# Kernel optimization log

Hardware: AMD Instinct MI355X
Metric: run time of the kernel (lower is better)

Reference implementation:

```python
import jax, jax.numpy as jnp
import numpy as np

B, T, V, H, E, MAX_OOV = 128, 200, 50257, 256, 128, 50


def setup_inputs() -> dict:
    key = jax.random.key(0)
    ks = jax.random.split(key, 17)
    s = 0.05  # param scale
    return {
        "decoder_input": jax.random.randint(ks[0], (B, 1), 0, V),
        "encoder_outputs": jax.random.normal(ks[1], (B, T, 2 * H), jnp.float32),
        "encoder_idxs": jax.random.randint(ks[2], (B, T), 0, V),
        "prev_state": jax.random.normal(ks[3], (1, B, H), jnp.float32),
        "selective_read": jax.random.normal(ks[4], (B, 1, 2 * H), jnp.float32) * s,
        "step": 1,
        "emb": jax.random.normal(ks[5], (V, E), jnp.float32) * s,
        "W_ih": jax.random.normal(ks[6], (3 * H, E + 2 * H), jnp.float32) * s,
        "W_hh": jax.random.normal(ks[7], (3 * H, H), jnp.float32) * s,
        "b_ih": jax.random.normal(ks[8], (3 * H,), jnp.float32) * s,
        "b_hh": jax.random.normal(ks[9], (3 * H,), jnp.float32) * s,
        "Wi_w": jax.random.normal(ks[10], (H, 2 * H), jnp.float32) * s,
        "Wi_b": jax.random.normal(ks[11], (H,), jnp.float32) * s,
        "Wg_w": jax.random.normal(ks[12], (V, H), jnp.float32) * s,
        "Wg_b": jax.random.normal(ks[13], (V,), jnp.float32) * s,
        "Wc_w": jax.random.normal(ks[14], (H, 2 * H), jnp.float32) * s,
        "Wc_b": jax.random.normal(ks[15], (H,), jnp.float32) * s,
    }


def _gru_cell(x, h, W_ih, W_hh, b_ih, b_hh):
    # torch GRUCell math, gate order r,z,n
    gi = x @ W_ih.T + b_ih
    gh = h @ W_hh.T + b_hh
    i_r, i_z, i_n = jnp.split(gi, 3, axis=-1)
    h_r, h_z, h_n = jnp.split(gh, 3, axis=-1)
    r = jax.nn.sigmoid(i_r + h_r)
    z = jax.nn.sigmoid(i_z + h_z)
    n = jnp.tanh(i_n + r * h_n)
    return (1.0 - z) * n + z * h


def reference(decoder_input, encoder_outputs, encoder_idxs, prev_state, selective_read,
              step, emb, W_ih, W_hh, b_ih, b_hh, Wi_w, Wi_b, Wg_w, Wg_b, Wc_w, Wc_b):
    dtype = encoder_outputs.dtype
    if step == 0:
        prev_state = (encoder_outputs[:, -1] @ Wi_w.T + Wi_b)[None]      # 1,B,H
        selective_read = jnp.zeros((B, 1, 2 * H), dtype)
    embedded = emb[decoder_input[:, 0]]                                   # B,E
    gru_in = jnp.concatenate([selective_read[:, 0], embedded], axis=-1)   # B,2H+E
    decode_hidden = _gru_cell(gru_in, prev_state[0], W_ih, W_hh, b_ih, b_hh)  # B,H

    score_g = decode_hidden @ Wg_w.T + Wg_b                               # B,V
    enc_proj = jnp.tanh(jnp.einsum('bte,he->bth', encoder_outputs, Wc_w) + Wc_b)  # B,T,H
    score_c = jnp.tanh(jnp.einsum('bth,bh->bt', enc_proj, decode_hidden))         # B,T
    score_c = score_c + jnp.where(encoder_idxs == 0, -10000.0, 0.0).astype(dtype)

    probs = jax.nn.softmax(jnp.concatenate([score_g, score_c], axis=1), axis=1)   # B,V+T
    prob_g, prob_c = probs[:, :V], probs[:, V:]
    prob_g = jnp.concatenate([prob_g, jnp.full((B, MAX_OOV), 1e-4, dtype)], axis=1)  # B,V+oov

    # copy-distribution aggregation: scatter-add prob_c by vocab id (replaces one-hot bmm)
    prob_c_to_g = jnp.zeros((B, V + MAX_OOV), dtype).at[
        jnp.arange(B)[:, None], encoder_idxs].add(prob_c)
    prob_out = (prob_c_to_g + prob_g)[:, None, :]                          # B,1,V+oov

    # selective read for next step
    match = (encoder_idxs == decoder_input).astype(dtype)                  # B,T
    tot = match.sum(axis=1, keepdims=True)
    match = jnp.where(tot > 1, match / tot, match)
    prob_appeared = prob_c * match
    selective_read_new = jnp.einsum('bt,bte->be', prob_appeared, encoder_outputs)[:, None, :]  # B,1,2H
    return prob_out, decode_hidden, selective_read_new
```

## Files before the change

kernel.cpp:

```cpp
#include <hip/hip_runtime.h>

typedef __bf16 bf16;
typedef __bf16 bf16x4 __attribute__((ext_vector_type(4)));
typedef __bf16 bf16x8 __attribute__((ext_vector_type(8)));
typedef float f32x4 __attribute__((ext_vector_type(4)));

#define B_ 128
#define T_ 200
#define V_ 50257
#define H_ 256
#define E_ 128
#define OOV_ 50
#define VO_ 50307
#define NRG 64
#define NTS 4
#define GSC 786
#define PSTR 800
#define GPJ 400

__device__ __forceinline__ float sigmoid_(float x) { return 1.0f / (1.0f + __expf(-x)); }
__device__ __forceinline__ float tanh_(float x) { return 1.0f - 2.0f / (__expf(2.0f * x) + 1.0f); }

__global__ void k_front(const float* Wc_w, bf16* WcPack,
                        const int* step_p, const float* enc, const float* prev,
                        const float* selread, const int* dec, const float* emb,
                        const float* Wi_w, const float* Wi_b,
                        float* hT, float* ginT) {
    if (blockIdx.x < 128) {
        int gid = blockIdx.x * 256 + threadIdx.x;
        int n = gid >> 7;
        int k = (gid & 127) * 4;
        float4 v = *(const float4*)(Wc_w + n * 512 + k);
        int kstep = k >> 5, kin = k & 31;
        int q = kin >> 3, j0 = kin & 7;
        int r = n & 15, nt = n >> 4;
        int lane = q * 16 + r;
        bf16* d = WcPack + (((nt * 16 + kstep) * 64) + lane) * 8 + j0;
        d[0] = (bf16)v.x; d[1] = (bf16)v.y; d[2] = (bf16)v.z; d[3] = (bf16)v.w;
    } else {
        int b = blockIdx.x - 128, t = threadIdx.x;
        int step = step_p[0];
        float h;
        if (step == 0) {
            float acc = Wi_b[t];
            const float* er = enc + (b * T_ + (T_ - 1)) * 512;
            const float* wr = Wi_w + t * 512;
            for (int k = 0; k < 512; ++k) acc += er[k] * wr[k];
            h = acc;
        } else {
            h = prev[b * H_ + t];
        }
        hT[t * B_ + b] = h;
        for (int k = t; k < 512; k += 256)
            ginT[k * B_ + b] = (step == 0) ? 0.0f : selread[b * 512 + k];
        if (t < E_)
            ginT[(512 + t) * B_ + b] = emb[dec[b] * E_ + t];
    }
}

__global__ void k_gemm_gru(const float* W_ih, const float* b_ih,
                           const float* W_hh, const float* b_hh,
                           const float* ginT, const float* hT,
                           float* giT, float* ghT) {
    __shared__ float red[256];
    int rrow = blockIdx.x;
    int t = threadIdx.x;
    int b = t & 127, kh = t >> 7;
    const float* w = W_ih + rrow * 640 + kh * 320;
    const float* g = ginT + (kh * 320) * B_ + b;
    float a0 = 0.f, a1 = 0.f, a2 = 0.f, a3 = 0.f;
#pragma unroll 4
    for (int k = 0; k < 320; k += 4) {
        a0 += w[k]     * g[k * B_];
        a1 += w[k + 1] * g[(k + 1) * B_];
        a2 += w[k + 2] * g[(k + 2) * B_];
        a3 += w[k + 3] * g[(k + 3) * B_];
    }
    const float* w2 = W_hh + rrow * 256 + kh * 128;
    const float* hh = hT + (kh * 128) * B_ + b;
    float c0 = 0.f, c1 = 0.f, c2 = 0.f, c3 = 0.f;
#pragma unroll 4
    for (int k = 0; k < 128; k += 4) {
        c0 += w2[k]     * hh[k * B_];
        c1 += w2[k + 1] * hh[(k + 1) * B_];
        c2 += w2[k + 2] * hh[(k + 2) * B_];
        c3 += w2[k + 3] * hh[(k + 3) * B_];
    }
    red[t] = ((a0 + a1) + (a2 + a3));
    __syncthreads();
    if (kh == 0) giT[rrow * B_ + b] = b_ih[rrow] + red[b] + red[b + 128];
    __syncthreads();
    red[t] = ((c0 + c1) + (c2 + c3));
    __syncthreads();
    if (kh == 0) ghT[rrow * B_ + b] = b_hh[rrow] + red[b] + red[b + 128];
}

__global__ void k_gru_cell(const float* giT, const float* ghT, const float* hT,
                           float* out_dh, bf16* Apack) {
    int b = blockIdx.x, j = threadIdx.x;
    float ir = giT[j * B_ + b], iz = giT[(256 + j) * B_ + b], in_ = giT[(512 + j) * B_ + b];
    float hr = ghT[j * B_ + b], hz = ghT[(256 + j) * B_ + b], hn = ghT[(512 + j) * B_ + b];
    float hp = hT[j * B_ + b];
    float r = sigmoid_(ir + hr);
    float z = sigmoid_(iz + hz);
    float n = tanh_(in_ + r * hn);
    float h = (1.0f - z) * n + z * hp;
    out_dh[b * H_ + j] = h;
    int mt = b >> 4, rr = b & 15, ks = j >> 5, q = (j >> 3) & 3, jj = j & 7;
    Apack[(((mt * 8 + ks) * 64) + (q * 16 + rr)) * 8 + jj] = (bf16)h;
}

__global__ __launch_bounds__(256, 4) void k_mm(const bf16* Apack, const float* Wg_w,
                                               const float* Wg_b, const float* enc,
                                               const bf16* WcPack, const float* Wc_b,
                                               const float* dh, const int* idxs,
                                               float* out_prob, float* pg_part, float* expc) {
    __shared__ unsigned char smem[34816];
    int tid = threadIdx.x;
    int w = tid >> 6, lane = tid & 63;
    int r = lane & 15, q = lane >> 4;
    if (blockIdx.x < GSC) {
        int blk = blockIdx.x;
        int n0 = blk * NRG;
        bf16* Bs = (bf16*)smem;
        float4 tmp[16];
#pragma unroll
        for (int j = 0; j < 16; ++j) {
            int f = j * 256 + tid;
            int row = f >> 6, c4 = f & 63;
            int n = n0 + row;
            tmp[j] = (n < V_) ? *(const float4*)(Wg_w + n * 256 + c4 * 4)
                              : float4{0.f, 0.f, 0.f, 0.f};
        }
#pragma unroll
        for (int j = 0; j < 16; ++j) {
            int f = j * 256 + tid;
            int row = f >> 6, c4 = f & 63;
            bf16x4 o;
            o[0] = (bf16)tmp[j].x; o[1] = (bf16)tmp[j].y;
            o[2] = (bf16)tmp[j].z; o[3] = (bf16)tmp[j].w;
            *(bf16x4*)(Bs + row * 264 + c4 * 4) = o;
        }
        bf16x8 a[2][8];
#pragma unroll
        for (int p = 0; p < 2; ++p)
#pragma unroll
            for (int ks = 0; ks < 8; ++ks)
                a[p][ks] = *(const bf16x8*)(Apack + ((2 * w + p) * 8 + ks) * 512 + lane * 8);
        __syncthreads();
        f32x4 acc[8];
#pragma unroll
        for (int i = 0; i < 8; ++i) acc[i] = (f32x4){0.f, 0.f, 0.f, 0.f};
#pragma unroll
        for (int ks = 0; ks < 8; ++ks) {
#pragma unroll
            for (int nt = 0; nt < NTS; ++nt) {
                bf16x8 bfr = *(const bf16x8*)(Bs + (nt * 16 + r) * 264 + ks * 32 + q * 8);
                acc[nt * 2]     = __builtin_amdgcn_mfma_f32_16x16x32_bf16(a[0][ks], bfr, acc[nt * 2], 0, 0, 0);
                acc[nt * 2 + 1] = __builtin_amdgcn_mfma_f32_16x16x32_bf16(a[1][ks], bfr, acc[nt * 2 + 1], 0, 0, 0);
            }
        }
        __syncthreads();
        float* Tr = (float*)smem;
        float rsum[2][4];
#pragma unroll
        for (int p = 0; p < 2; ++p)
#pragma unroll
            for (int rg = 0; rg < 4; ++rg) rsum[p][rg] = 0.0f;
#pragma unroll
        for (int nt = 0; nt < NTS; ++nt) {
            int n = n0 + nt * 16 + r;
            bool valid = n < V_;
            float wgb = valid ? Wg_b[n] : 0.0f;
#pragma unroll
            for (int p = 0; p < 2; ++p) {
#pragma unroll
                for (int rg = 0; rg < 4; ++rg) {
                    int row = (2 * w + p) * 16 + q * 4 + rg;
                    float e = valid ? __expf(acc[nt * 2 + p][rg] + wgb) : 0.0f;
                    Tr[row * 68 + nt * 16 + r] = e;
                    rsum[p][rg] += e;
                }
            }
        }
#pragma unroll
        for (int p = 0; p < 2; ++p) {
#pragma unroll
            for (int rg = 0; rg < 4; ++rg) {
                float s = rsum[p][rg];
                s += __shfl_xor(s, 1);
                s += __shfl_xor(s, 2);
                s += __shfl_xor(s, 4);
                s += __shfl_xor(s, 8);
                if (r == 0) {
                    int row = (2 * w + p) * 16 + q * 4 + rg;
                    pg_part[row * PSTR + blk] = s;
                }
            }
        }
        __syncthreads();
        if (blk < GSC - 1) {
#pragma unroll
            for (int rnd = 0; rnd < 8; ++rnd) {
                int f = rnd * 256 + tid;
                int row = f >> 4;
                int c4 = f & 15;
                float4 v = *(const float4*)(Tr + row * 68 + c4 * 4);
                *(float4*)(out_prob + row * VO_ + n0 + c4 * 4) = v;
            }
        } else {
#pragma unroll
            for (int rnd = 0; rnd < 8; ++rnd) {
                int f = rnd * 256 + tid;
                int row = f >> 4;
                int c4 = f & 15;
#pragma unroll
                for (int i = 0; i < 4; ++i) {
                    int n = n0 + c4 * 4 + i;
                    if (n < V_) out_prob[row * VO_ + n] = Tr[row * 68 + c4 * 4 + i];
                }
            }
        }
    } else {
        int pblk = blockIdx.x - GSC;
        int m0 = pblk * 64;
        bf16* As = (bf16*)smem;
        float* sred = (float*)(smem + 33792);
        f32x4 acc[16];
#pragma unroll
        for (int i = 0; i < 16; ++i) acc[i] = (f32x4){0.f, 0.f, 0.f, 0.f};
        for (int half = 0; half < 2; ++half) {
            __syncthreads();
            float4 tmp[16];
#pragma unroll
            for (int j = 0; j < 16; ++j) {
                int f = j * 256 + tid;
                int row = f >> 6, c4 = f & 63;
                tmp[j] = *(const float4*)(enc + (m0 + row) * 512 + half * 256 + c4 * 4);
            }
#pragma unroll
            for (int j = 0; j < 16; ++j) {
                int f = j * 256 + tid;
                int row = f >> 6, c4 = f & 63;
                bf16x4 o;
                o[0] = (bf16)tmp[j].x; o[1] = (bf16)tmp[j].y;
                o[2] = (bf16)tmp[j].z; o[3] = (bf16)tmp[j].w;
                *(bf16x4*)(As + row * 264 + c4 * 4) = o;
            }
            __syncthreads();
#pragma unroll
            for (int ks = 0; ks < 8; ++ks) {
                int kstep = half * 8 + ks;
                bf16x8 bfr[4];
#pragma unroll
                for (int ntl = 0; ntl < 4; ++ntl)
                    bfr[ntl] = *(const bf16x8*)(WcPack + (((w * 4 + ntl) * 16 + kstep) * 64 + lane) * 8);
#pragma unroll
                for (int mt = 0; mt < 4; ++mt) {
                    bf16x8 a = *(const bf16x8*)(As + (mt * 16 + r) * 264 + ks * 32 + q * 8);
#pragma unroll
                    for (int ntl = 0; ntl < 4; ++ntl)
                        acc[mt * 4 + ntl] = __builtin_amdgcn_mfma_f32_16x16x32_bf16(a, bfr[ntl], acc[mt * 4 + ntl], 0, 0, 0);
                }
            }
        }
#pragma unroll
        for (int mt = 0; mt < 4; ++mt) {
#pragma unroll
            for (int rg = 0; rg < 4; ++rg) {
                int rowl = mt * 16 + q * 4 + rg;
                int row = m0 + rowl;
                int b = row / T_;
                float s = 0.0f;
#pragma unroll
                for (int ntl = 0; ntl < 4; ++ntl) {
                    int n = (w * 4 + ntl) * 16 + r;
                    float pv = tanh_(acc[mt * 4 + ntl][rg] + Wc_b[n]);
                    s += pv * dh[b * H_ + n];
                }
                s += __shfl_xor(s, 1);
                s += __shfl_xor(s, 2);
                s += __shfl_xor(s, 4);
                s += __shfl_xor(s, 8);
                if (r == 0) sred[rowl * 4 + w] = s;
            }
        }
        __syncthreads();
        if (tid < 64) {
            float s = sred[tid * 4] + sred[tid * 4 + 1] + sred[tid * 4 + 2] + sred[tid * 4 + 3];
            int row = m0 + tid;
            int b = row / T_, t = row - b * T_;
            float sc = tanh_(s);
            if (idxs[b * T_ + t] == 0) sc -= 10000.0f;
            expc[row] = __expf(sc);
        }
    }
}

__global__ void k_red_scatter(const float* pg_part, const float* expc_, const int* idxs,
                              const int* dec, const float* enc, float* inv_out,
                              float* out_prob, float* out_sel) {
    __shared__ float red[256];
    __shared__ float cf[256];
    int b = blockIdx.x, t = threadIdx.x;
    float s = 0.0f;
    for (int i = t; i < GSC; i += 256) s += pg_part[b * PSTR + i];
    if (t < T_) s += expc_[b * T_ + t];
    red[t] = s;
    __syncthreads();
    for (int k = 128; k > 0; k >>= 1) {
        if (t < k) red[t] += red[t + k];
        __syncthreads();
    }
    float iv = 1.0f / red[0];
    if (t == 0) inv_out[b] = iv;
    __syncthreads();
    int d = dec[b];
    float ec = 0.0f;
    int m = 0;
    if (t < T_) {
        int ix = idxs[b * T_ + t];
        ec = expc_[b * T_ + t];
        atomicAdd(&out_prob[b * VO_ + ix], ec);
        m = (ix == d) ? 1 : 0;
    }
    cf[t] = m ? ec * iv : 0.0f;
    red[t] = m ? 1.0f : 0.0f;
    __syncthreads();
    for (int k = 128; k > 0; k >>= 1) {
        if (t < k) red[t] += red[t + k];
        __syncthreads();
    }
    float tot = red[0];
    float scale = (tot > 1.0f) ? 1.0f / tot : 1.0f;
    float a0 = 0.0f, a1 = 0.0f;
    for (int tt = 0; tt < T_; ++tt) {
        float c = cf[tt];
        if (c != 0.0f) {
            float wgt = c * scale;
            a0 += wgt * enc[(b * T_ + tt) * 512 + t];
            a1 += wgt * enc[(b * T_ + tt) * 512 + t + 256];
        }
    }
    out_sel[b * 512 + t] = a0;
    out_sel[b * 512 + t + 256] = a1;
}

__global__ void k_norm(float* out_prob, const float* inv) {
    int i4 = blockIdx.x * 256 + threadIdx.x;
    if (i4 >= (B_ * VO_ / 4)) return;
    float4 vv = ((const float4*)out_prob)[i4];
    float r[4];
    int base = i4 * 4;
#pragma unroll
    for (int c = 0; c < 4; ++c) {
        int idx = base + c;
        int b = idx / VO_;
        int v = idx - b * VO_;
        float x = (c == 0) ? vv.x : (c == 1) ? vv.y : (c == 2) ? vv.z : vv.w;
        r[c] = (v < V_) ? x * inv[b] : 1e-4f;
    }
    ((float4*)out_prob)[i4] = make_float4(r[0], r[1], r[2], r[3]);
}

extern "C" void kernel_launch(void* const* d_in, const int* in_sizes, int n_in,
                              void* d_out, int out_size, void* d_ws, size_t ws_size,
                              hipStream_t stream) {
    const int*   dec     = (const int*)d_in[0];
    const float* enc     = (const float*)d_in[1];
    const int*   idxs    = (const int*)d_in[2];
    const float* prev    = (const float*)d_in[3];
    const float* selread = (const float*)d_in[4];
    const int*   step_p  = (const int*)d_in[5];
    const float* emb     = (const float*)d_in[6];
    const float* W_ih    = (const float*)d_in[7];
    const float* W_hh    = (const float*)d_in[8];
    const float* b_ih    = (const float*)d_in[9];
    const float* b_hh    = (const float*)d_in[10];
    const float* Wi_w    = (const float*)d_in[11];
    const float* Wi_b    = (const float*)d_in[12];
    const float* Wg_w    = (const float*)d_in[13];
    const float* Wg_b    = (const float*)d_in[14];
    const float* Wc_w    = (const float*)d_in[15];
    const float* Wc_b    = (const float*)d_in[16];

    float* ws     = (float*)d_ws;
    float* hT     = ws;
    float* ginT   = ws + 32768;
    float* giT    = ws + 114688;
    float* ghT    = ws + 212992;
    float* inv    = ws + 311296;
    float* expc   = ws + 311552;
    float* pgp    = ws + 337152;
    bf16*  Apack  = (bf16*)(ws + 741376);
    bf16*  WcPack = (bf16*)(ws + 757760);

    float* out      = (float*)d_out;
    float* out_prob = out;
    float* out_dh   = out + 6439296;
    float* out_sel  = out + 6439296 + 32768;

    k_front<<<256, 256, 0, stream>>>(Wc_w, WcPack, step_p, enc, prev, selread, dec,
                                     emb, Wi_w, Wi_b, hT, ginT);
    k_gemm_gru<<<768, 256, 0, stream>>>(W_ih, b_ih, W_hh, b_hh, ginT, hT, giT, ghT);
    k_gru_cell<<<B_, 256, 0, stream>>>(giT, ghT, hT, out_dh, Apack);
    k_mm<<<GSC + GPJ, 256, 0, stream>>>(Apack, Wg_w, Wg_b, enc, WcPack, Wc_b,
                                        out_dh, idxs, out_prob, pgp, expc);
    k_red_scatter<<<B_, 256, 0, stream>>>(pgp, expc, idxs, dec, enc, inv, out_prob, out_sel);
    k_norm<<<(B_ * VO_ / 4 + 255) / 256, 256, 0, stream>>>(out_prob, inv);
}
```

Baseline: 282.3 us.

## Fuse normalization into scatter kernel and load Wg directly into MFMA fragments

The separate normalization kernel is removed. Each batch row is now split across two blocks in the reduce/scatter kernel, which scatter-adds the copy probabilities into its half of the vocabulary and then rescales that half in place, and also computes half of the selective-read dimensions. The vocabulary GEMM now converts Wg_w straight from global memory into bf16 MFMA B fragments with a one-step register prefetch, skipping the shared-memory staging. It uses 80-row tiles with launch bounds lowered to 3, and writes exp values directly to the output instead of through a shared transpose. This cuts a launch and a full extra pass over the large output, at the cost of uncoalesced scattered stores and more register pressure.

```diff
diff --git a/kernel.cpp b/kernel.cpp
--- a/kernel.cpp
+++ b/kernel.cpp
@@ -12,10 +12,10 @@
 #define E_ 128
 #define OOV_ 50
 #define VO_ 50307
-#define NRG 64
-#define NTS 4
-#define GSC 786
-#define PSTR 800
+#define NRG 80
+#define NTS 5
+#define GSC 629
+#define PSTR 640
 #define GPJ 400
 
 __device__ __forceinline__ float sigmoid_(float x) { return 1.0f / (1.0f + __expf(-x)); }
@@ -110,7 +110,7 @@
     Apack[(((mt * 8 + ks) * 64) + (q * 16 + rr)) * 8 + jj] = (bf16)h;
 }
 
-__global__ __launch_bounds__(256, 4) void k_mm(const bf16* Apack, const float* Wg_w,
+__global__ __launch_bounds__(256, 3) void k_mm(const bf16* Apack, const float* Wg_w,
                                                const float* Wg_b, const float* enc,
                                                const bf16* WcPack, const float* Wc_b,
                                                const float* dh, const int* idxs,
@@ -122,64 +122,68 @@
     if (blockIdx.x < GSC) {
         int blk = blockIdx.x;
         int n0 = blk * NRG;
-        bf16* Bs = (bf16*)smem;
-        float4 tmp[16];
-#pragma unroll
-        for (int j = 0; j < 16; ++j) {
-            int f = j * 256 + tid;
-            int row = f >> 6, c4 = f & 63;
-            int n = n0 + row;
-            tmp[j] = (n < V_) ? *(const float4*)(Wg_w + n * 256 + c4 * 4)
-                              : float4{0.f, 0.f, 0.f, 0.f};
-        }
-#pragma unroll
-        for (int j = 0; j < 16; ++j) {
-            int f = j * 256 + tid;
-            int row = f >> 6, c4 = f & 63;
-            bf16x4 o;
-            o[0] = (bf16)tmp[j].x; o[1] = (bf16)tmp[j].y;
-            o[2] = (bf16)tmp[j].z; o[3] = (bf16)tmp[j].w;
-            *(bf16x4*)(Bs + row * 264 + c4 * 4) = o;
-        }
-        bf16x8 a[2][8];
-#pragma unroll
-        for (int p = 0; p < 2; ++p)
-#pragma unroll
-            for (int ks = 0; ks < 8; ++ks)
-                a[p][ks] = *(const bf16x8*)(Apack + ((2 * w + p) * 8 + ks) * 512 + lane * 8);
-        __syncthreads();
-        f32x4 acc[8];
-#pragma unroll
-        for (int i = 0; i < 8; ++i) acc[i] = (f32x4){0.f, 0.f, 0.f, 0.f};
-#pragma unroll
-        for (int ks = 0; ks < 8; ++ks) {
-#pragma unroll
-            for (int nt = 0; nt < NTS; ++nt) {
-                bf16x8 bfr = *(const bf16x8*)(Bs + (nt * 16 + r) * 264 + ks * 32 + q * 8);
-                acc[nt * 2]     = __builtin_amdgcn_mfma_f32_16x16x32_bf16(a[0][ks], bfr, acc[nt * 2], 0, 0, 0);
-                acc[nt * 2 + 1] = __builtin_amdgcn_mfma_f32_16x16x32_bf16(a[1][ks], bfr, acc[nt * 2 + 1], 0, 0, 0);
-            }
-        }
-        __syncthreads();
-        float* Tr = (float*)smem;
-        float rsum[2][4];
-#pragma unroll
-        for (int p = 0; p < 2; ++p)
-#pragma unroll
-            for (int rg = 0; rg < 4; ++rg) rsum[p][rg] = 0.0f;
+        const float* rp[NTS];
+        bool valid[NTS];
+        int nrow[NTS];
 #pragma unroll
         for (int nt = 0; nt < NTS; ++nt) {
             int n = n0 + nt * 16 + r;
-            bool valid = n < V_;
-            float wgb = valid ? Wg_b[n] : 0.0f;
+            valid[nt] = (n < V_);
+            nrow[nt] = valid[nt] ? n : (V_ - 1);
+            rp[nt] = Wg_w + nrow[nt] * 256 + q * 8;
+        }
+        f32x4 acc[10];
+#pragma unroll
+        for (int i = 0; i < 10; ++i) acc[i] = (f32x4){0.f, 0.f, 0.f, 0.f};
+        float4 vA[NTS], vB[NTS];
+#pragma unroll
+        for (int nt = 0; nt < NTS; ++nt) {
+            vA[nt] = *(const float4*)(rp[nt]);
+            vB[nt] = *(const float4*)(rp[nt] + 4);
+        }
+#pragma unroll
+        for (int ks = 0; ks < 8; ++ks) {
+            bf16x8 bfr[NTS];
+#pragma unroll
+            for (int nt = 0; nt < NTS; ++nt) {
+                float4 va = vA[nt], vb = vB[nt];
+                bfr[nt][0] = (bf16)va.x; bfr[nt][1] = (bf16)va.y;
+                bfr[nt][2] = (bf16)va.z; bfr[nt][3] = (bf16)va.w;
+                bfr[nt][4] = (bf16)vb.x; bfr[nt][5] = (bf16)vb.y;
+                bfr[nt][6] = (bf16)vb.z; bfr[nt][7] = (bf16)vb.w;
+            }
+            if (ks < 7) {
+#pragma unroll
+                for (int nt = 0; nt < NTS; ++nt) {
+                    vA[nt] = *(const float4*)(rp[nt] + (ks + 1) * 32);
+                    vB[nt] = *(const float4*)(rp[nt] + (ks + 1) * 32 + 4);
+                }
+            }
+            bf16x8 a0 = *(const bf16x8*)(Apack + ((2 * w + 0) * 8 + ks) * 512 + lane * 8);
+            bf16x8 a1 = *(const bf16x8*)(Apack + ((2 * w + 1) * 8 + ks) * 512 + lane * 8);
+#pragma unroll
+            for (int nt = 0; nt < NTS; ++nt) {
+                acc[nt * 2]     = __builtin_amdgcn_mfma_f32_16x16x32_bf16(a0, bfr[nt], acc[nt * 2], 0, 0, 0);
+                acc[nt * 2 + 1] = __builtin_amdgcn_mfma_f32_16x16x32_bf16(a1, bfr[nt], acc[nt * 2 + 1], 0, 0, 0);
+            }
+        }
+        float rsum[2][4];
+#pragma unroll
+        for (int p = 0; p < 2; ++p)
+#pragma unroll
+            for (int rg = 0; rg < 4; ++rg) rsum[p][rg] = 0.0f;
+#pragma unroll
+        for (int nt = 0; nt < NTS; ++nt) {
+            float wgb = Wg_b[nrow[nt]];
+            int n = n0 + nt * 16 + r;
 #pragma unroll
             for (int p = 0; p < 2; ++p) {
 #pragma unroll
                 for (int rg = 0; rg < 4; ++rg) {
                     int row = (2 * w + p) * 16 + q * 4 + rg;
-                    float e = valid ? __expf(acc[nt * 2 + p][rg] + wgb) : 0.0f;
-                    Tr[row * 68 + nt * 16 + r] = e;
+                    float e = valid[nt] ? __expf(acc[nt * 2 + p][rg] + wgb) : 0.0f;
                     rsum[p][rg] += e;
+                    if (valid[nt]) out_prob[row * VO_ + n] = e;
                 }
             }
         }
@@ -198,29 +202,6 @@
                 }
             }
         }
-        __syncthreads();
-        if (blk < GSC - 1) {
-#pragma unroll
-            for (int rnd = 0; rnd < 8; ++rnd) {
-                int f = rnd * 256 + tid;
-                int row = f >> 4;
-                int c4 = f & 15;
-                float4 v = *(const float4*)(Tr + row * 68 + c4 * 4);
-                *(float4*)(out_prob + row * VO_ + n0 + c4 * 4) = v;
-            }
-        } else {
-#pragma unroll
-            for (int rnd = 0; rnd < 8; ++rnd) {
-                int f = rnd * 256 + tid;
-                int row = f >> 4;
-                int c4 = f & 15;
-#pragma unroll
-                for (int i = 0; i < 4; ++i) {
-                    int n = n0 + c4 * 4 + i;
-                    if (n < V_) out_prob[row * VO_ + n] = Tr[row * 68 + c4 * 4 + i];
-                }
-            }
-        }
     } else {
         int pblk = blockIdx.x - GSC;
         int m0 = pblk * 64;
@@ -231,21 +212,24 @@
         for (int i = 0; i < 16; ++i) acc[i] = (f32x4){0.f, 0.f, 0.f, 0.f};
         for (int half = 0; half < 2; ++half) {
             __syncthreads();
-            float4 tmp[16];
-#pragma unroll
-            for (int j = 0; j < 16; ++j) {
-                int f = j * 256 + tid;
-                int row = f >> 6, c4 = f & 63;
-                tmp[j] = *(const float4*)(enc + (m0 + row) * 512 + half * 256 + c4 * 4);
-            }
-#pragma unroll
-            for (int j = 0; j < 16; ++j) {
-                int f = j * 256 + tid;
-                int row = f >> 6, c4 = f & 63;
-                bf16x4 o;
-                o[0] = (bf16)tmp[j].x; o[1] = (bf16)tmp[j].y;
-                o[2] = (bf16)tmp[j].z; o[3] = (bf16)tmp[j].w;
-                *(bf16x4*)(As + row * 264 + c4 * 4) = o;
+#pragma unroll
+            for (int ph = 0; ph < 2; ++ph) {
+                float4 tmp[8];
+#pragma unroll
+                for (int j = 0; j < 8; ++j) {
+                    int f = (ph * 8 + j) * 256 + tid;
+                    int row = f >> 6, c4 = f & 63;
+                    tmp[j] = *(const float4*)(enc + (m0 + row) * 512 + half * 256 + c4 * 4);
+                }
+#pragma unroll
+                for (int j = 0; j < 8; ++j) {
+                    int f = (ph * 8 + j) * 256 + tid;
+                    int row = f >> 6, c4 = f & 63;
+                    bf16x4 o;
+                    o[0] = (bf16)tmp[j].x; o[1] = (bf16)tmp[j].y;
+                    o[2] = (bf16)tmp[j].z; o[3] = (bf16)tmp[j].w;
+                    *(bf16x4*)(As + row * 264 + c4 * 4) = o;
+                }
             }
             __syncthreads();
 #pragma unroll
@@ -298,11 +282,12 @@
 }
 
 __global__ void k_red_scatter(const float* pg_part, const float* expc_, const int* idxs,
-                              const int* dec, const float* enc, float* inv_out,
+                              const int* dec, const float* enc,
                               float* out_prob, float* out_sel) {
     __shared__ float red[256];
     __shared__ float cf[256];
-    int b = blockIdx.x, t = threadIdx.x;
+    int b = blockIdx.x >> 1, hf = blockIdx.x & 1;
+    int t = threadIdx.x;
     float s = 0.0f;
     for (int i = t; i < GSC; i += 256) s += pg_part[b * PSTR + i];
     if (t < T_) s += expc_[b * T_ + t];
@@ -313,15 +298,18 @@
         __syncthreads();
     }
     float iv = 1.0f / red[0];
-    if (t == 0) inv_out[b] = iv;
     __syncthreads();
     int d = dec[b];
+    const int halfc = (VO_ + 1) / 2;
+    int cl0 = hf * halfc;
+    int cl1 = (cl0 + halfc < VO_) ? cl0 + halfc : VO_;
     float ec = 0.0f;
     int m = 0;
     if (t < T_) {
         int ix = idxs[b * T_ + t];
         ec = expc_[b * T_ + t];
-        atomicAdd(&out_prob[b * VO_ + ix], ec);
+        if (ix >= cl0 && ix < cl1)
+            atomicAdd(&out_prob[b * VO_ + ix], ec);
         m = (ix == d) ? 1 : 0;
     }
     cf[t] = m ? ec * iv : 0.0f;
@@ -333,34 +321,39 @@
     }
     float tot = red[0];
     float scale = (tot > 1.0f) ? 1.0f / tot : 1.0f;
-    float a0 = 0.0f, a1 = 0.0f;
+    int dim = t + hf * 256;
+    float a0 = 0.0f;
     for (int tt = 0; tt < T_; ++tt) {
         float c = cf[tt];
-        if (c != 0.0f) {
-            float wgt = c * scale;
-            a0 += wgt * enc[(b * T_ + tt) * 512 + t];
-            a1 += wgt * enc[(b * T_ + tt) * 512 + t + 256];
-        }
-    }
-    out_sel[b * 512 + t] = a0;
-    out_sel[b * 512 + t + 256] = a1;
-}
-
-__global__ void k_norm(float* out_prob, const float* inv) {
-    int i4 = blockIdx.x * 256 + threadIdx.x;
-    if (i4 >= (B_ * VO_ / 4)) return;
-    float4 vv = ((const float4*)out_prob)[i4];
-    float r[4];
-    int base = i4 * 4;
-#pragma unroll
-    for (int c = 0; c < 4; ++c) {
-        int idx = base + c;
-        int b = idx / VO_;
-        int v = idx - b * VO_;
-        float x = (c == 0) ? vv.x : (c == 1) ? vv.y : (c == 2) ? vv.z : vv.w;
-        r[c] = (v < V_) ? x * inv[b] : 1e-4f;
-    }
-    ((float4*)out_prob)[i4] = make_float4(r[0], r[1], r[2], r[3]);
+        if (c != 0.0f) a0 += c * scale * enc[(b * T_ + tt) * 512 + dim];
+    }
+    out_sel[b * 512 + dim] = a0;
+    __threadfence();
+    __syncthreads();
+    int base = b * VO_;
+    int s0 = base + cl0, s1 = base + cl1;
+    int a4 = (s0 + 3) & ~3;
+    int b4 = s1 & ~3;
+    if (t < a4 - s0) {
+        int i = s0 + t;
+        int col = i - base;
+        out_prob[i] = (col < V_) ? out_prob[i] * iv : 1e-4f;
+    }
+    if (t < s1 - b4) {
+        int i = b4 + t;
+        int col = i - base;
+        out_prob[i] = (col < V_) ? out_prob[i] * iv : 1e-4f;
+    }
+    for (int i4 = a4 / 4 + t; i4 < b4 / 4; i4 += 256) {
+        float4 v = *(const float4*)(out_prob + i4 * 4);
+        int c0 = i4 * 4 - base;
+        float o[4];
+        o[0] = (c0 + 0 < V_) ? v.x * iv : 1e-4f;
+        o[1] = (c0 + 1 < V_) ? v.y * iv : 1e-4f;
+        o[2] = (c0 + 2 < V_) ? v.z * iv : 1e-4f;
+        o[3] = (c0 + 3 < V_) ? v.w * iv : 1e-4f;
+        *(float4*)(out_prob + i4 * 4) = make_float4(o[0], o[1], o[2], o[3]);
+    }
 }
 
 extern "C" void kernel_launch(void* const* d_in, const int* in_sizes, int n_in,
@@ -389,7 +382,6 @@
     float* ginT   = ws + 32768;
     float* giT    = ws + 114688;
     float* ghT    = ws + 212992;
-    float* inv    = ws + 311296;
     float* expc   = ws + 311552;
     float* pgp    = ws + 337152;
     bf16*  Apack  = (bf16*)(ws + 741376);
@@ -406,6 +398,5 @@
     k_gru_cell<<<B_, 256, 0, stream>>>(giT, ghT, hT, out_dh, Apack);
     k_mm<<<GSC + GPJ, 256, 0, stream>>>(Apack, Wg_w, Wg_b, enc, WcPack, Wc_b,
                                         out_dh, idxs, out_prob, pgp, expc);
-    k_red_scatter<<<B_, 256, 0, stream>>>(pgp, expc, idxs, dec, enc, inv, out_prob, out_sel);
-    k_norm<<<(B_ * VO_ / 4 + 255) / 256, 256, 0, stream>>>(out_prob, inv);
-}
+    k_red_scatter<<<256, 256, 0, stream>>>(pgp, expc, idxs, dec, enc, out_prob, out_sel);
+}
```

After: 279.6 us. No clear change (-1.0%).

## Split fused GEMM kernel; load Wg directly into registers without LDS staging

Applied to the files above, without the earlier changes.

The merged k_mm kernel is split into two launches, k_proj and k_score. k_score now loads fp32 Wg_w rows straight from global memory into MFMA B fragments with two-stage register double buffering, and writes exp scores directly to global memory instead of staging them through LDS. This removes the shared-memory round trips and barriers, and lets more score blocks stay resident. In exchange it adds a second kernel launch and serialises the projection and score phases. The direct stores are scalar and strided, which may coalesce poorly, and each lane reads 32-byte chunks across separate rows.

```diff
diff --git a/kernel.cpp b/kernel.cpp
--- a/kernel.cpp
+++ b/kernel.cpp
@@ -110,190 +110,180 @@
     Apack[(((mt * 8 + ks) * 64) + (q * 16 + rr)) * 8 + jj] = (bf16)h;
 }
 
-__global__ __launch_bounds__(256, 4) void k_mm(const bf16* Apack, const float* Wg_w,
-                                               const float* Wg_b, const float* enc,
-                                               const bf16* WcPack, const float* Wc_b,
-                                               const float* dh, const int* idxs,
-                                               float* out_prob, float* pg_part, float* expc) {
+__global__ __launch_bounds__(256, 3) void k_score(const bf16* Apack, const float* Wg_w,
+                                                  const float* Wg_b,
+                                                  float* out_prob, float* pg_part) {
+    int tid = threadIdx.x;
+    int w = tid >> 6, lane = tid & 63;
+    int r = lane & 15, q = lane >> 4;
+    int blk = blockIdx.x;
+    int n0 = blk * NRG;
+    int off[NTS];
+#pragma unroll
+    for (int nt = 0; nt < NTS; ++nt) {
+        int n = n0 + nt * 16 + r;
+        off[nt] = ((n < V_) ? n : (V_ - 1)) * 256;
+    }
+    const float* bp = Wg_w + q * 8;
+    f32x4 acc[8];
+#pragma unroll
+    for (int i = 0; i < 8; ++i) acc[i] = (f32x4){0.f, 0.f, 0.f, 0.f};
+    float4 vA[2][NTS], vB[2][NTS];
+#pragma unroll
+    for (int nt = 0; nt < NTS; ++nt) {
+        vA[0][nt] = *(const float4*)(bp + off[nt]);
+        vB[0][nt] = *(const float4*)(bp + off[nt] + 4);
+    }
+#pragma unroll
+    for (int nt = 0; nt < NTS; ++nt) {
+        vA[1][nt] = *(const float4*)(bp + off[nt] + 32);
+        vB[1][nt] = *(const float4*)(bp + off[nt] + 36);
+    }
+#pragma unroll
+    for (int ks = 0; ks < 8; ++ks) {
+        int cur = ks & 1;
+        bf16x8 bfr[NTS];
+#pragma unroll
+        for (int nt = 0; nt < NTS; ++nt) {
+            float4 va = vA[cur][nt], vb = vB[cur][nt];
+            bfr[nt][0] = (bf16)va.x; bfr[nt][1] = (bf16)va.y;
+            bfr[nt][2] = (bf16)va.z; bfr[nt][3] = (bf16)va.w;
+            bfr[nt][4] = (bf16)vb.x; bfr[nt][5] = (bf16)vb.y;
+            bfr[nt][6] = (bf16)vb.z; bfr[nt][7] = (bf16)vb.w;
+        }
+        if (ks < 6) {
+#pragma unroll
+            for (int nt = 0; nt < NTS; ++nt) {
+                vA[cur][nt] = *(const float4*)(bp + off[nt] + (ks + 2) * 32);
+                vB[cur][nt] = *(const float4*)(bp + off[nt] + (ks + 2) * 32 + 4);
+            }
+        }
+        bf16x8 a0 = *(const bf16x8*)(Apack + ((2 * w + 0) * 8 + ks) * 512 + lane * 8);
+        bf16x8 a1 = *(const bf16x8*)(Apack + ((2 * w + 1) * 8 + ks) * 512 + lane * 8);
+#pragma unroll
+        for (int nt = 0; nt < NTS; ++nt) {
+            acc[nt * 2]     = __builtin_amdgcn_mfma_f32_16x16x32_bf16(a0, bfr[nt], acc[nt * 2], 0, 0, 0);
+            acc[nt * 2 + 1] = __builtin_amdgcn_mfma_f32_16x16x32_bf16(a1, bfr[nt], acc[nt * 2 + 1], 0, 0, 0);
+        }
+    }
+    float rsum[2][4];
+#pragma unroll
+    for (int p = 0; p < 2; ++p)
+#pragma unroll
+        for (int rg = 0; rg < 4; ++rg) rsum[p][rg] = 0.0f;
+#pragma unroll
+    for (int nt = 0; nt < NTS; ++nt) {
+        int n = n0 + nt * 16 + r;
+        bool valid = (n < V_);
+        float wgb = Wg_b[valid ? n : (V_ - 1)];
+#pragma unroll
+        for (int p = 0; p < 2; ++p) {
+#pragma unroll
+            for (int rg = 0; rg < 4; ++rg) {
+                int row = (2 * w + p) * 16 + q * 4 + rg;
+                float e = valid ? __expf(acc[nt * 2 + p][rg] + wgb) : 0.0f;
+                rsum[p][rg] += e;
+                if (valid) out_prob[row * VO_ + n] = e;
+            }
+        }
+    }
+#pragma unroll
+    for (int p = 0; p < 2; ++p) {
+#pragma unroll
+        for (int rg = 0; rg < 4; ++rg) {
+            float s = rsum[p][rg];
+            s += __shfl_xor(s, 1);
+            s += __shfl_xor(s, 2);
+            s += __shfl_xor(s, 4);
+            s += __shfl_xor(s, 8);
+            if (r == 0) {
+                int row = (2 * w + p) * 16 + q * 4 + rg;
+                pg_part[row * PSTR + blk] = s;
+            }
+        }
+    }
+}
+
+__global__ __launch_bounds__(256, 4) void k_proj(const float* enc, const bf16* WcPack,
+                                                 const float* Wc_b, const float* dh,
+                                                 const int* idxs, float* expc) {
     __shared__ unsigned char smem[34816];
     int tid = threadIdx.x;
     int w = tid >> 6, lane = tid & 63;
     int r = lane & 15, q = lane >> 4;
-    if (blockIdx.x < GSC) {
-        int blk = blockIdx.x;
-        int n0 = blk * NRG;
-        bf16* Bs = (bf16*)smem;
-        float4 tmp[16];
-#pragma unroll
-        for (int j = 0; j < 16; ++j) {
-            int f = j * 256 + tid;
-            int row = f >> 6, c4 = f & 63;
-            int n = n0 + row;
-            tmp[j] = (n < V_) ? *(const float4*)(Wg_w + n * 256 + c4 * 4)
-                              : float4{0.f, 0.f, 0.f, 0.f};
-        }
-#pragma unroll
-        for (int j = 0; j < 16; ++j) {
-            int f = j * 256 + tid;
-            int row = f >> 6, c4 = f & 63;
-            bf16x4 o;
-            o[0] = (bf16)tmp[j].x; o[1] = (bf16)tmp[j].y;
-            o[2] = (bf16)tmp[j].z; o[3] = (bf16)tmp[j].w;
-            *(bf16x4*)(Bs + row * 264 + c4 * 4) = o;
-        }
-        bf16x8 a[2][8];
-#pragma unroll
-        for (int p = 0; p < 2; ++p)
-#pragma unroll
-            for (int ks = 0; ks < 8; ++ks)
-                a[p][ks] = *(const bf16x8*)(Apack + ((2 * w + p) * 8 + ks) * 512 + lane * 8);
+    int m0 = blockIdx.x * 64;
+    bf16* As = (bf16*)smem;
+    float* sred = (float*)(smem + 33792);
+    f32x4 acc[16];
+#pragma unroll
+    for (int i = 0; i < 16; ++i) acc[i] = (f32x4){0.f, 0.f, 0.f, 0.f};
+    for (int half = 0; half < 2; ++half) {
         __syncthreads();
-        f32x4 acc[8];
-#pragma unroll
-        for (int i = 0; i < 8; ++i) acc[i] = (f32x4){0.f, 0.f, 0.f, 0.f};
-#pragma unroll
-        for (int ks = 0; ks < 8; ++ks) {
-#pragma unroll
-            for (int nt = 0; nt < NTS; ++nt) {
-                bf16x8 bfr = *(const bf16x8*)(Bs + (nt * 16 + r) * 264 + ks * 32 + q * 8);
-                acc[nt * 2]     = __builtin_amdgcn_mfma_f32_16x16x32_bf16(a[0][ks], bfr, acc[nt * 2], 0, 0, 0);
-                acc[nt * 2 + 1] = __builtin_amdgcn_mfma_f32_16x16x32_bf16(a[1][ks], bfr, acc[nt * 2 + 1], 0, 0, 0);
-            }
-        }
-        __syncthreads();
-        float* Tr = (float*)smem;
-        float rsum[2][4];
-#pragma unroll
-        for (int p = 0; p < 2; ++p)
-#pragma unroll
-            for (int rg = 0; rg < 4; ++rg) rsum[p][rg] = 0.0f;
-#pragma unroll
-        for (int nt = 0; nt < NTS; ++nt) {
-            int n = n0 + nt * 16 + r;
-            bool valid = n < V_;
-            float wgb = valid ? Wg_b[n] : 0.0f;
-#pragma unroll
-            for (int p = 0; p < 2; ++p) {
-#pragma unroll
-                for (int rg = 0; rg < 4; ++rg) {
-                    int row = (2 * w + p) * 16 + q * 4 + rg;
-                    float e = valid ? __expf(acc[nt * 2 + p][rg] + wgb) : 0.0f;
-                    Tr[row * 68 + nt * 16 + r] = e;
-                    rsum[p][rg] += e;
-                }
-            }
-        }
-#pragma unroll
-        for (int p = 0; p < 2; ++p) {
-#pragma unroll
-            for (int rg = 0; rg < 4; ++rg) {
-                float s = rsum[p][rg];
-                s += __shfl_xor(s, 1);
-                s += __shfl_xor(s, 2);
-                s += __shfl_xor(s, 4);
-                s += __shfl_xor(s, 8);
-                if (r == 0) {
-                    int row = (2 * w + p) * 16 + q * 4 + rg;
-                    pg_part[row * PSTR + blk] = s;
-                }
-            }
-        }
-        __syncthreads();
-        if (blk < GSC - 1) {
-#pragma unroll
-            for (int rnd = 0; rnd < 8; ++rnd) {
-                int f = rnd * 256 + tid;
-                int row = f >> 4;
-                int c4 = f & 15;
-                float4 v = *(const float4*)(Tr + row * 68 + c4 * 4);
-                *(float4*)(out_prob + row * VO_ + n0 + c4 * 4) = v;
-            }
-        } else {
-#pragma unroll
-            for (int rnd = 0; rnd < 8; ++rnd) {
-                int f = rnd * 256 + tid;
-                int row = f >> 4;
-                int c4 = f & 15;
-#pragma unroll
-                for (int i = 0; i < 4; ++i) {
-                    int n = n0 + c4 * 4 + i;
-                    if (n < V_) out_prob[row * VO_ + n] = Tr[row * 68 + c4 * 4 + i];
-                }
-            }
-        }
-    } else {
-        int pblk = blockIdx.x - GSC;
-        int m0 = pblk * 64;
-        bf16* As = (bf16*)smem;
-        float* sred = (float*)(smem + 33792);
-        f32x4 acc[16];
-#pragma unroll
-        for (int i = 0; i < 16; ++i) acc[i] = (f32x4){0.f, 0.f, 0.f, 0.f};
-        for (int half = 0; half < 2; ++half) {
-            __syncthreads();
-            float4 tmp[16];
-#pragma unroll
-            for (int j = 0; j < 16; ++j) {
-                int f = j * 256 + tid;
+#pragma unroll
+        for (int ph = 0; ph < 2; ++ph) {
+            float4 tmp[8];
+#pragma unroll
+            for (int j = 0; j < 8; ++j) {
+                int f = (ph * 8 + j) * 256 + tid;
                 int row = f >> 6, c4 = f & 63;
                 tmp[j] = *(const float4*)(enc + (m0 + row) * 512 + half * 256 + c4 * 4);
             }
 #pragma unroll
-            for (int j = 0; j < 16; ++j) {
-                int f = j * 256 + tid;
+            for (int j = 0; j < 8; ++j) {
+                int f = (ph * 8 + j) * 256 + tid;
                 int row = f >> 6, c4 = f & 63;
                 bf16x4 o;
                 o[0] = (bf16)tmp[j].x; o[1] = (bf16)tmp[j].y;
                 o[2] = (bf16)tmp[j].z; o[3] = (bf16)tmp[j].w;
                 *(bf16x4*)(As + row * 264 + c4 * 4) = o;
             }
-            __syncthreads();
-#pragma unroll
-            for (int ks = 0; ks < 8; ++ks) {
-                int kstep = half * 8 + ks;
-                bf16x8 bfr[4];
+        }
+        __syncthreads();
+#pragma unroll
+        for (int ks = 0; ks < 8; ++ks) {
+            int kstep = half * 8 + ks;
+            bf16x8 bfr[4];
+#pragma unroll
+            for (int ntl = 0; ntl < 4; ++ntl)
+                bfr[ntl] = *(const bf16x8*)(WcPack + (((w * 4 + ntl) * 16 + kstep) * 64 + lane) * 8);
+#pragma unroll
+            for (int mt = 0; mt < 4; ++mt) {
+                bf16x8 a = *(const bf16x8*)(As + (mt * 16 + r) * 264 + ks * 32 + q * 8);
 #pragma unroll
                 for (int ntl = 0; ntl < 4; ++ntl)
-                    bfr[ntl] = *(const bf16x8*)(WcPack + (((w * 4 + ntl) * 16 + kstep) * 64 + lane) * 8);
-#pragma unroll
-                for (int mt = 0; mt < 4; ++mt) {
-                    bf16x8 a = *(const bf16x8*)(As + (mt * 16 + r) * 264 + ks * 32 + q * 8);
-#pragma unroll
-                    for (int ntl = 0; ntl < 4; ++ntl)
-                        acc[mt * 4 + ntl] = __builtin_amdgcn_mfma_f32_16x16x32_bf16(a, bfr[ntl], acc[mt * 4 + ntl], 0, 0, 0);
-                }
-            }
-        }
-#pragma unroll
-        for (int mt = 0; mt < 4; ++mt) {
-#pragma unroll
-            for (int rg = 0; rg < 4; ++rg) {
-                int rowl = mt * 16 + q * 4 + rg;
-                int row = m0 + rowl;
-                int b = row / T_;
-                float s = 0.0f;
-#pragma unroll
-                for (int ntl = 0; ntl < 4; ++ntl) {
-                    int n = (w * 4 + ntl) * 16 + r;
-                    float pv = tanh_(acc[mt * 4 + ntl][rg] + Wc_b[n]);
-                    s += pv * dh[b * H_ + n];
-                }
-                s += __shfl_xor(s, 1);
-                s += __shfl_xor(s, 2);
-                s += __shfl_xor(s, 4);
-                s += __shfl_xor(s, 8);
-                if (r == 0) sred[rowl * 4 + w] = s;
-            }
-        }
-        __syncthreads();
-        if (tid < 64) {
-            float s = sred[tid * 4] + sred[tid * 4 + 1] + sred[tid * 4 + 2] + sred[tid * 4 + 3];
-            int row = m0 + tid;
-            int b = row / T_, t = row - b * T_;
-            float sc = tanh_(s);
-            if (idxs[b * T_ + t] == 0) sc -= 10000.0f;
-            expc[row] = __expf(sc);
-        }
+                    acc[mt * 4 + ntl] = __builtin_amdgcn_mfma_f32_16x16x32_bf16(a, bfr[ntl], acc[mt * 4 + ntl], 0, 0, 0);
+            }
+        }
+    }
+#pragma unroll
+    for (int mt = 0; mt < 4; ++mt) {
+#pragma unroll
+        for (int rg = 0; rg < 4; ++rg) {
+            int rowl = mt * 16 + q * 4 + rg;
+            int row = m0 + rowl;
+            int b = row / T_;
+            float s = 0.0f;
+#pragma unroll
+            for (int ntl = 0; ntl < 4; ++ntl) {
+                int n = (w * 4 + ntl) * 16 + r;
+                float pv = tanh_(acc[mt * 4 + ntl][rg] + Wc_b[n]);
+                s += pv * dh[b * H_ + n];
+            }
+            s += __shfl_xor(s, 1);
+            s += __shfl_xor(s, 2);
+            s += __shfl_xor(s, 4);
+            s += __shfl_xor(s, 8);
+            if (r == 0) sred[rowl * 4 + w] = s;
+        }
+    }
+    __syncthreads();
+    if (tid < 64) {
+        float s = sred[tid * 4] + sred[tid * 4 + 1] + sred[tid * 4 + 2] + sred[tid * 4 + 3];
+        int row = m0 + tid;
+        int b = row / T_, t = row - b * T_;
+        float sc = tanh_(s);
+        if (idxs[b * T_ + t] == 0) sc -= 10000.0f;
+        expc[row] = __expf(sc);
     }
 }
 
@@ -404,8 +394,8 @@
                                      emb, Wi_w, Wi_b, hT, ginT);
     k_gemm_gru<<<768, 256, 0, stream>>>(W_ih, b_ih, W_hh, b_hh, ginT, hT, giT, ghT);
     k_gru_cell<<<B_, 256, 0, stream>>>(giT, ghT, hT, out_dh, Apack);
-    k_mm<<<GSC + GPJ, 256, 0, stream>>>(Apack, Wg_w, Wg_b, enc, WcPack, Wc_b,
-                                        out_dh, idxs, out_prob, pgp, expc);
+    k_proj<<<GPJ, 256, 0, stream>>>(enc, WcPack, Wc_b, out_dh, idxs, expc);
+    k_score<<<GSC, 256, 0, stream>>>(Apack, Wg_w, Wg_b, out_prob, pgp);
     k_red_scatter<<<B_, 256, 0, stream>>>(pgp, expc, idxs, dec, enc, inv, out_prob, out_sel);
     k_norm<<<(B_ * VO_ / 4 + 255) / 256, 256, 0, stream>>>(out_prob, inv);
 }
```

After: 298.9 us. 1.06x slower.
